# Optimization experiments

Measured on AMD Instinct MI355X. Metric: run time of the kernel, lower is better.

## Reference

```python
import jax, jax.numpy as jnp
import numpy as np

D = 512      # model dim
H = 8        # heads
HD = D // H  # head dim = 64
NQ = 2048    # n_query
NC = 4096    # n_context
EPS = 1e-5   # LayerNorm eps (torch default)


def setup_inputs() -> dict:
    key = jax.random.key(0)
    ks = jax.random.split(key, 12)
    s = 0.02
    return {
        "query_repr": jax.random.normal(ks[0], (NQ, D), dtype=jnp.float32),
        "context_repr": jax.random.normal(ks[1], (NC, D), dtype=jnp.float32),
        "query_coords": jax.random.uniform(ks[2], (NQ, 2), dtype=jnp.float32) * 10.0,
        "context_coords": jax.random.uniform(ks[3], (NC, 2), dtype=jnp.float32) * 10.0,
        "Wq": jax.random.normal(ks[4], (D, D), dtype=jnp.float32) * s,
        "bq": jnp.zeros((D,), jnp.float32),
        "Wk": jax.random.normal(ks[5], (D, D), dtype=jnp.float32) * s,
        "bk": jnp.zeros((D,), jnp.float32),
        "Wv": jax.random.normal(ks[6], (D, D), dtype=jnp.float32) * s,
        "bv": jnp.zeros((D,), jnp.float32),
        "Wo": jax.random.normal(ks[7], (D, D), dtype=jnp.float32) * s,
        "bo": jnp.zeros((D,), jnp.float32),
        "ln_g": jnp.ones((D,), jnp.float32),
        "ln_b": jnp.zeros((D,), jnp.float32),
        "log_scale": jnp.array(0.0, jnp.float32),          # log_distance_scale
        "bias_per_head": jnp.ones((H,), jnp.float32),      # distance_bias_per_head
    }


def reference(query_repr, context_repr, query_coords, context_coords,
              Wq, bq, Wk, bk, Wv, bv, Wo, bo, ln_g, ln_b,
              log_scale, bias_per_head):
    # pairwise Euclidean distances (NQ, NC)
    diff = query_coords[:, None, :] - context_coords[None, :, :]
    dist = jnp.sqrt(jnp.sum(diff * diff, axis=-1))
    # per-head additive attention bias (H, NQ, NC)
    bias = (-jnp.exp(log_scale) * dist)[None, :, :] * bias_per_head[:, None, None]

    # multi-head attention (batch=1, eval mode so dropout is identity)
    q = (query_repr @ Wq.T + bq).reshape(NQ, H, HD).transpose(1, 0, 2)    # (H, NQ, HD)
    k = (context_repr @ Wk.T + bk).reshape(NC, H, HD).transpose(1, 0, 2)  # (H, NC, HD)
    v = (context_repr @ Wv.T + bv).reshape(NC, H, HD).transpose(1, 0, 2)  # (H, NC, HD)

    scale = 1.0 / jnp.sqrt(jnp.float32(HD))
    scores = jnp.einsum('hqd,hkd->hqk', q, k) * scale + bias              # (H, NQ, NC)
    attn = jax.nn.softmax(scores, axis=-1)
    ctx = jnp.einsum('hqk,hkd->hqd', attn, v)                             # (H, NQ, HD)
    attended = ctx.transpose(1, 0, 2).reshape(NQ, D) @ Wo.T + bo          # (NQ, D)

    # residual + LayerNorm
    x = attended + query_repr
    mu = jnp.mean(x, axis=-1, keepdims=True)
    var = jnp.mean((x - mu) ** 2, axis=-1, keepdims=True)
    return (x - mu) / jnp.sqrt(var + EPS) * ln_g + ln_b
```

## Files before the change

kernel.cpp:

```cpp
#include <hip/hip_runtime.h>

#define D 512
#define H 8
#define HD 64
#define NQ 2048
#define NC 4096
#define SPLIT 8
#define CLEN (NC / SPLIT)
#define NT (CLEN / 32)
#define M0 3.0f
#define KP2 136
#define VP 40

#define TBM 128
#define TBN 64
#define TBK 32
#define TPAD 40

typedef __attribute__((ext_vector_type(8))) short short8;
typedef __attribute__((ext_vector_type(4))) short short4v;
typedef __attribute__((ext_vector_type(4))) float float4v;
typedef __attribute__((ext_vector_type(4))) int int4v;

__device__ inline float bf2f(short s) {
    unsigned int u = ((unsigned int)(unsigned short)s) << 16;
    return __builtin_bit_cast(float, u);
}
__device__ inline short f2bf(float f) {
    unsigned int u = __builtin_bit_cast(unsigned int, f);
    u = (u + 0x7FFF + ((u >> 16) & 1)) >> 16;
    return (short)u;
}
__device__ inline int cvtpk(float a, float b) {
    int w;
    asm("v_cvt_pk_bf16_f32 %0, %1, %2" : "=v"(w) : "v"(a), "v"(b));
    return w;
}

__global__ __launch_bounds__(256) void cast_all(
    const float* __restrict__ s0, const float* __restrict__ s1,
    const float* __restrict__ s2, const float* __restrict__ s3,
    const float* __restrict__ s4, const float* __restrict__ s5,
    short* __restrict__ dst)
{
    int i = blockIdx.x * 256 + threadIdx.x;
    const float* src; int off;
    if      (i < 262144) { src = s0; off = i; }
    else if (i < 786432) { src = s1; off = i - 262144; }
    else if (i < 851968) { src = s2; off = i - 786432; }
    else if (i < 917504) { src = s3; off = i - 851968; }
    else if (i < 983040) { src = s4; off = i - 917504; }
    else                 { src = s5; off = i - 983040; }
    float4v v = ((const float4v*)src)[off];
    short4v o;
    o.x = f2bf(v.x); o.y = f2bf(v.y); o.z = f2bf(v.z); o.w = f2bf(v.w);
    ((short4v*)dst)[i] = o;
}

__global__ __launch_bounds__(256) void gemm_bt_bias(
    const short* __restrict__ X, const short* __restrict__ W,
    const float* __restrict__ bias, short* __restrict__ out, int M)
{
    int wave = threadIdx.x >> 6, lane = threadIdx.x & 63;
    int gt = blockIdx.x * 4 + wave;
    int tm = gt >> 3;
    int tg = gt & 7;
    if (tm >= (M >> 4)) return;
    int l15 = lane & 15, quad = lane >> 4;
    const short* xp = X + (tm * 16 + l15) * D + quad * 8;
    const short* wp = W + (tg * 64 + l15) * D + quad * 8;
    float4v a0 = {0,0,0,0}, a1 = {0,0,0,0}, a2 = {0,0,0,0}, a3 = {0,0,0,0};
#pragma unroll
    for (int k = 0; k < D; k += 32) {
        short8 a  = *(const short8*)(xp + k);
        short8 b0 = *(const short8*)(wp + k);
        short8 b1 = *(const short8*)(wp + 16 * D + k);
        short8 b2 = *(const short8*)(wp + 32 * D + k);
        short8 b3 = *(const short8*)(wp + 48 * D + k);
        a0 = __builtin_amdgcn_mfma_f32_16x16x32_bf16(a, b0, a0, 0, 0, 0);
        a1 = __builtin_amdgcn_mfma_f32_16x16x32_bf16(a, b1, a1, 0, 0, 0);
        a2 = __builtin_amdgcn_mfma_f32_16x16x32_bf16(a, b2, a2, 0, 0, 0);
        a3 = __builtin_amdgcn_mfma_f32_16x16x32_bf16(a, b3, a3, 0, 0, 0);
    }
    int orow = tm * 16 + quad * 4;
    float4v accs[4] = {a0, a1, a2, a3};
#pragma unroll
    for (int j = 0; j < 4; j++) {
        int col = tg * 64 + j * 16 + l15;
        float bv = bias[col];
#pragma unroll
        for (int r = 0; r < 4; r++)
            out[(orow + r) * D + col] = f2bf(accs[j][r] + bv);
    }
}

__global__ __launch_bounds__(256) void gemm_qkv_tiled(
    const short* __restrict__ Xq, const short* __restrict__ Xc,
    const short* __restrict__ Wq, const short* __restrict__ Wk,
    const short* __restrict__ Wv,
    const float* __restrict__ bq, const float* __restrict__ bk,
    const float* __restrict__ bv,
    short* __restrict__ Qout, short* __restrict__ Kout,
    short* __restrict__ VoutT)
{
    __shared__ __align__(16) short Ab[2][TBM * TPAD];
    __shared__ __align__(16) short Bb[2][TBN * TPAD];

    int tid = threadIdx.x;
    int wave = tid >> 6, lane = tid & 63;
    int quad = lane >> 4, l15 = lane & 15;

    int blk = blockIdx.x;
    const short *X, *W;
    const float* bias;
    short* outp;
    int bm, bn, vmode;
    if (blk < 128) {
        X = Xq; W = Wq; bias = bq; outp = Qout; vmode = 0;
        bm = (blk >> 3) * TBM; bn = (blk & 7) * TBN;
    } else if (blk < 384) {
        int b = blk - 128;
        X = Xc; W = Wk; bias = bk; outp = Kout; vmode = 0;
        bm = (b >> 3) * TBM; bn = (b & 7) * TBN;
    } else {
        int b = blk - 384;
        X = Xc; W = Wv; bias = bv; outp = VoutT; vmode = 1;
        bm = (b >> 3) * TBM; bn = (b & 7) * TBN;
    }

    int ar = tid >> 1, ac = (tid & 1) * 16;
    int br = tid >> 2, bc = (tid & 3) * 8;
    const short* ag = X + (size_t)(bm + ar) * D + ac;
    const short* bg = W + (size_t)(bn + br) * D + bc;
    short* aw0 = &Ab[0][ar * TPAD + ac];
    short* aw1 = &Ab[1][ar * TPAD + ac];
    short* bw0 = &Bb[0][br * TPAD + bc];
    short* bw1 = &Bb[1][br * TPAD + bc];

    short8 ra0, ra1, rb;

#define GLOAD(ks) { const short* ap_ = ag + (ks) * TBK;                        \
        ra0 = *(const short8*)(ap_);                                           \
        ra1 = *(const short8*)(ap_ + 8);                                       \
        rb  = *(const short8*)(bg + (ks) * TBK); }
#define GDSW0 { *(short8*)aw0 = ra0; *(short8*)(aw0 + 8) = ra1;                \
                *(short8*)bw0 = rb; }
#define GDSW1 { *(short8*)aw1 = ra0; *(short8*)(aw1 + 8) = ra1;                \
                *(short8*)bw1 = rb; }

    float4v c00 = {0,0,0,0}, c01 = {0,0,0,0}, c02 = {0,0,0,0}, c03 = {0,0,0,0};
    float4v c10 = {0,0,0,0}, c11 = {0,0,0,0}, c12 = {0,0,0,0}, c13 = {0,0,0,0};

#define GCOMP(B)                                                               \
    {                                                                          \
        const short* abase = &Ab[B][(wave * 32 + l15) * TPAD + quad * 8];      \
        const short* bbase = &Bb[B][l15 * TPAD + quad * 8];                    \
        short8 a0 = *(const short8*)(abase);                                   \
        short8 a1 = *(const short8*)(abase + 16 * TPAD);                       \
        short8 b0 = *(const short8*)(bbase);                                   \
        short8 b1 = *(const short8*)(bbase + 16 * TPAD);                       \
        short8 b2 = *(const short8*)(bbase + 32 * TPAD);                       \
        short8 b3 = *(const short8*)(bbase + 48 * TPAD);                       \
        c00 = __builtin_amdgcn_mfma_f32_16x16x32_bf16(a0, b0, c00, 0, 0, 0);   \
        c01 = __builtin_amdgcn_mfma_f32_16x16x32_bf16(a0, b1, c01, 0, 0, 0);   \
        c02 = __builtin_amdgcn_mfma_f32_16x16x32_bf16(a0, b2, c02, 0, 0, 0);   \
        c03 = __builtin_amdgcn_mfma_f32_16x16x32_bf16(a0, b3, c03, 0, 0, 0);   \
        c10 = __builtin_amdgcn_mfma_f32_16x16x32_bf16(a1, b0, c10, 0, 0, 0);   \
        c11 = __builtin_amdgcn_mfma_f32_16x16x32_bf16(a1, b1, c11, 0, 0, 0);   \
        c12 = __builtin_amdgcn_mfma_f32_16x16x32_bf16(a1, b2, c12, 0, 0, 0);   \
        c13 = __builtin_amdgcn_mfma_f32_16x16x32_bf16(a1, b3, c13, 0, 0, 0);   \
    }

    GLOAD(0);
    GDSW0;
    GLOAD(1);
    __syncthreads();

    for (int t = 0; t < 14; t += 2) {
        GDSW1;
        GLOAD(t + 2);
        GCOMP(0);
        __syncthreads();
        GDSW0;
        GLOAD(t + 3);
        GCOMP(1);
        __syncthreads();
    }
    GDSW1;
    GCOMP(0);
    __syncthreads();
    GCOMP(1);

#undef GLOAD
#undef GDSW0
#undef GDSW1
#undef GCOMP

    float4v accs[2][4] = {{c00, c01, c02, c03}, {c10, c11, c12, c13}};
    if (vmode == 0) {
#pragma unroll
        for (int mf = 0; mf < 2; mf++) {
            int orow = bm + wave * 32 + mf * 16 + quad * 4;
#pragma unroll
            for (int nf = 0; nf < 4; nf++) {
                int col = bn + nf * 16 + l15;
                float bb_ = bias[col];
#pragma unroll
                for (int r = 0; r < 4; r++)
                    outp[(size_t)(orow + r) * D + col] = f2bf(accs[mf][nf][r] + bb_);
            }
        }
    } else {
#pragma unroll
        for (int mf = 0; mf < 2; mf++) {
            int orow = bm + wave * 32 + mf * 16 + quad * 4;
            int a = (orow & 31) >> 2;
            int posb = (a < 4) ? (8 * a) : (8 * (a - 4) + 4);
            int cp = (orow & ~31) + posb;
#pragma unroll
            for (int nf = 0; nf < 4; nf++) {
                int col = bn + nf * 16 + l15;
                float bb_ = bias[col];
                short4v o;
#pragma unroll
                for (int r = 0; r < 4; r++) o[r] = f2bf(accs[mf][nf][r] + bb_);
                *(short4v*)(outp + (size_t)col * NC + cp) = o;
            }
        }
    }
}

__global__ __launch_bounds__(256) void gemm_res_ln(
    const short* __restrict__ X, const short* __restrict__ W,
    const float* __restrict__ bias, const float* __restrict__ resid,
    const float* __restrict__ g, const float* __restrict__ b,
    float* __restrict__ out)
{
    __shared__ float redS[4][4][4];
    __shared__ float redV[4][4][4];

    int wave = threadIdx.x >> 6, lane = threadIdx.x & 63;
    int l15 = lane & 15, quad = lane >> 4;
    int tm = blockIdx.x;
    const short* xp  = X + (tm * 16 + l15) * D + quad * 8;
    const short* wp0 = W + ((2 * wave) * 64 + l15) * D + quad * 8;
    const short* wp1 = wp0 + 64 * D;
    float4v a00 = {0,0,0,0}, a01 = {0,0,0,0}, a02 = {0,0,0,0}, a03 = {0,0,0,0};
    float4v a10 = {0,0,0,0}, a11 = {0,0,0,0}, a12 = {0,0,0,0}, a13 = {0,0,0,0};
#pragma unroll
    for (int k = 0; k < D; k += 32) {
        short8 a   = *(const short8*)(xp + k);
        short8 b00 = *(const short8*)(wp0 + k);
        short8 b01 = *(const short8*)(wp0 + 16 * D + k);
        short8 b02 = *(const short8*)(wp0 + 32 * D + k);
        short8 b03 = *(const short8*)(wp0 + 48 * D + k);
        short8 b10 = *(const short8*)(wp1 + k);
        short8 b11 = *(const short8*)(wp1 + 16 * D + k);
        short8 b12 = *(const short8*)(wp1 + 32 * D + k);
        short8 b13 = *(const short8*)(wp1 + 48 * D + k);
        a00 = __builtin_amdgcn_mfma_f32_16x16x32_bf16(a, b00, a00, 0, 0, 0);
        a01 = __builtin_amdgcn_mfma_f32_16x16x32_bf16(a, b01, a01, 0, 0, 0);
        a02 = __builtin_amdgcn_mfma_f32_16x16x32_bf16(a, b02, a02, 0, 0, 0);
        a03 = __builtin_amdgcn_mfma_f32_16x16x32_bf16(a, b03, a03, 0, 0, 0);
        a10 = __builtin_amdgcn_mfma_f32_16x16x32_bf16(a, b10, a10, 0, 0, 0);
        a11 = __builtin_amdgcn_mfma_f32_16x16x32_bf16(a, b11, a11, 0, 0, 0);
        a12 = __builtin_amdgcn_mfma_f32_16x16x32_bf16(a, b12, a12, 0, 0, 0);
        a13 = __builtin_amdgcn_mfma_f32_16x16x32_bf16(a, b13, a13, 0, 0, 0);
    }
    int orow = tm * 16 + quad * 4;
    float v[2][4][4];
    float4v accs[2][4] = {{a00, a01, a02, a03}, {a10, a11, a12, a13}};
#pragma unroll
    for (int t = 0; t < 2; t++) {
#pragma unroll
        for (int j = 0; j < 4; j++) {
            int col = (2 * wave + t) * 64 + j * 16 + l15;
            float bv = bias[col];
#pragma unroll
            for (int r = 0; r < 4; r++)
                v[t][j][r] = accs[t][j][r] + bv + resid[(orow + r) * D + col];
        }
    }
    float ps[4];
#pragma unroll
    for (int r = 0; r < 4; r++) {
        float s = 0.f;
#pragma unroll
        for (int t = 0; t < 2; t++)
#pragma unroll
            for (int j = 0; j < 4; j++) s += v[t][j][r];
#pragma unroll
        for (int off = 1; off < 16; off <<= 1) s += __shfl_xor(s, off);
        ps[r] = s;
    }
    if (l15 == 0) {
#pragma unroll
        for (int r = 0; r < 4; r++) redS[wave][quad][r] = ps[r];
    }
    __syncthreads();
    float mu[4];
#pragma unroll
    for (int r = 0; r < 4; r++)
        mu[r] = (redS[0][quad][r] + redS[1][quad][r] +
                 redS[2][quad][r] + redS[3][quad][r]) * (1.f / D);
#pragma unroll
    for (int r = 0; r < 4; r++) {
        float s = 0.f;
#pragma unroll
        for (int t = 0; t < 2; t++)
#pragma unroll
            for (int j = 0; j < 4; j++) {
                float d = v[t][j][r] - mu[r];
                s += d * d;
            }
#pragma unroll
        for (int off = 1; off < 16; off <<= 1) s += __shfl_xor(s, off);
        ps[r] = s;
    }
    if (l15 == 0) {
#pragma unroll
        for (int r = 0; r < 4; r++) redV[wave][quad][r] = ps[r];
    }
    __syncthreads();
    float rstd[4];
#pragma unroll
    for (int r = 0; r < 4; r++) {
        float var = (redV[0][quad][r] + redV[1][quad][r] +
                     redV[2][quad][r] + redV[3][quad][r]) * (1.f / D);
        rstd[r] = rsqrtf(var + 1e-5f);
    }
#pragma unroll
    for (int t = 0; t < 2; t++) {
#pragma unroll
        for (int j = 0; j < 4; j++) {
            int col = (2 * wave + t) * 64 + j * 16 + l15;
            float gc = g[col], bc = b[col];
#pragma unroll
            for (int r = 0; r < 4; r++)
                out[(orow + r) * D + col] =
                    (v[t][j][r] - mu[r]) * rstd[r] * gc + bc;
        }
    }
}

__global__ __launch_bounds__(256) void gemm_bt_bias_res_f32(
    const short* __restrict__ X, const short* __restrict__ W,
    const float* __restrict__ bias, const float* __restrict__ resid,
    float* __restrict__ out, int M)
{
    int wave = threadIdx.x >> 6, lane = threadIdx.x & 63;
    int gt = blockIdx.x * 4 + wave;
    int tm = gt >> 3;
    int tg = gt & 7;
    if (tm >= (M >> 4)) return;
    int l15 = lane & 15, quad = lane >> 4;
    const short* xp = X + (tm * 16 + l15) * D + quad * 8;
    const short* wp = W + (tg * 64 + l15) * D + quad * 8;
    float4v a0 = {0,0,0,0}, a1 = {0,0,0,0}, a2 = {0,0,0,0}, a3 = {0,0,0,0};
#pragma unroll
    for (int k = 0; k < D; k += 32) {
        short8 a  = *(const short8*)(xp + k);
        short8 b0 = *(const short8*)(wp + k);
        short8 b1 = *(const short8*)(wp + 16 * D + k);
        short8 b2 = *(const short8*)(wp + 32 * D + k);
        short8 b3 = *(const short8*)(wp + 48 * D + k);
        a0 = __builtin_amdgcn_mfma_f32_16x16x32_bf16(a, b0, a0, 0, 0, 0);
        a1 = __builtin_amdgcn_mfma_f32_16x16x32_bf16(a, b1, a1, 0, 0, 0);
        a2 = __builtin_amdgcn_mfma_f32_16x16x32_bf16(a, b2, a2, 0, 0, 0);
        a3 = __builtin_amdgcn_mfma_f32_16x16x32_bf16(a, b3, a3, 0, 0, 0);
    }
    int orow = tm * 16 + quad * 4;
    float4v accs[4] = {a0, a1, a2, a3};
#pragma unroll
    for (int j = 0; j < 4; j++) {
        int col = tg * 64 + j * 16 + l15;
        float bv = bias[col];
#pragma unroll
        for (int r = 0; r < 4; r++) {
            int q = orow + r;
            out[q * D + col] = accs[j][r] + bv + resid[q * D + col];
        }
    }
}

__global__ __launch_bounds__(256) void attn_mfma_split9(
    const short* __restrict__ Q, const short* __restrict__ K,
    const short* __restrict__ Vp,
    const float* __restrict__ qc, const float* __restrict__ cc,
    const float* __restrict__ log_scale, const float* __restrict__ bph,
    short* __restrict__ Opart, float* __restrict__ Lpart)
{
    __shared__ __align__(16) short Klds[2][32 * KP2];
    __shared__ __align__(16) short Vlds[2][128 * VP];
    __shared__ __align__(16) float ccl[512];

    int tid = threadIdx.x;
    int wave = tid >> 6, lane = tid & 63;
    int h0 = blockIdx.y * 2;
    int sp = blockIdx.z;
    int q0 = blockIdx.x * 64 + wave * 16;
    int quad = lane >> 4, l15 = lane & 15;
    int cbase = sp * CLEN;

    const float LOG2E = 1.4426950408889634f;
    const float escale = 0.125f * LOG2E;
    const float M0L = M0 * LOG2E;
    float ebase = __expf(log_scale[0]);
    float bh0 = ebase * bph[h0] * LOG2E;
    float bh1 = ebase * bph[h0 + 1] * LOG2E;

    const short* qp = Q + (q0 + l15) * D + h0 * HD + quad * 8;
    short8 qa0_0 = *(const short8*)(qp);
    short8 qa1_0 = *(const short8*)(qp + 32);
    short8 qa0_1 = *(const short8*)(qp + 64);
    short8 qa1_1 = *(const short8*)(qp + 96);

    float qx = qc[(q0 + l15) * 2];
    float qy = qc[(q0 + l15) * 2 + 1];

    float lacc0 = 0.f, lacc1 = 0.f;
    float4v O00 = {0,0,0,0}, O01 = {0,0,0,0}, O02 = {0,0,0,0}, O03 = {0,0,0,0};
    float4v O10 = {0,0,0,0}, O11 = {0,0,0,0}, O12 = {0,0,0,0}, O13 = {0,0,0,0};

    int kr_ = tid >> 3, kc_ = tid & 7;
    int vr_ = tid >> 2, vc_ = tid & 3;
    const short* kg  = K + (size_t)h0 * HD + kc_ * 8;
    const short* vg0 = Vp + (size_t)(h0 * HD + vr_) * NC + vc_ * 8;
    const short* vg1 = Vp + (size_t)(h0 * HD + 64 + vr_) * NC + vc_ * 8;
    short* kw0a = &Klds[0][kr_ * KP2 + kc_ * 8];
    short* kw1a = &Klds[1][kr_ * KP2 + kc_ * 8];
    short* vw0a = &Vlds[0][vr_ * VP + vc_ * 8];
    short* vw0b = &Vlds[0][(64 + vr_) * VP + vc_ * 8];
    short* vw1a = &Vlds[1][vr_ * VP + vc_ * 8];
    short* vw1b = &Vlds[1][(64 + vr_) * VP + vc_ * 8];

    short8 rka, rkb, rva, rvb;

#define LOADR(c0_)                                                             \
    {                                                                          \
        const short* kp_ = kg + (size_t)((c0_) + kr_) * D;                     \
        rka = *(const short8*)(kp_);                                           \
        rkb = *(const short8*)(kp_ + 64);                                      \
        rva = *(const short8*)(vg0 + (c0_));                                   \
        rvb = *(const short8*)(vg1 + (c0_));                                   \
    }

#define DSW0 { *(short8*)kw0a = rka; *(short8*)(kw0a + 64) = rkb;              \
               *(short8*)vw0a = rva; *(short8*)vw0b = rvb; }
#define DSW1 { *(short8*)kw1a = rka; *(short8*)(kw1a + 64) = rkb;              \
               *(short8*)vw1a = rva; *(short8*)vw1b = rvb; }

    const float2* ccp = (const float2*)ccl;

#define HEAD(hoff, QA0, QA1, BH, LACC, OA, OB, OC, OD)                         \
    {                                                                          \
        short8 k00 = *(const short8*)(kb + l15 * KP2 + (hoff) + quad * 8);     \
        short8 k01 = *(const short8*)(kb + l15 * KP2 + (hoff) + 32 + quad * 8);\
        short8 k10 = *(const short8*)(kb + (16 + l15) * KP2 + (hoff) + quad * 8);\
        short8 k11 = *(const short8*)(kb + (16 + l15) * KP2 + (hoff) + 32 + quad * 8);\
        float4v s0 = {0,0,0,0}, s1 = {0,0,0,0};                                \
        s0 = __builtin_amdgcn_mfma_f32_16x16x32_bf16(k00, QA0, s0, 0, 0, 0);   \
        s0 = __builtin_amdgcn_mfma_f32_16x16x32_bf16(k01, QA1, s0, 0, 0, 0);   \
        s1 = __builtin_amdgcn_mfma_f32_16x16x32_bf16(k10, QA0, s1, 0, 0, 0);   \
        s1 = __builtin_amdgcn_mfma_f32_16x16x32_bf16(k11, QA1, s1, 0, 0, 0);   \
        short8 v0 = *(const short8*)(vb + ((hoff) / 64 * 64 + l15) * VP + quad * 8);       \
        short8 v1 = *(const short8*)(vb + ((hoff) / 64 * 64 + 16 + l15) * VP + quad * 8);  \
        short8 v2 = *(const short8*)(vb + ((hoff) / 64 * 64 + 32 + l15) * VP + quad * 8);  \
        short8 v3 = *(const short8*)(vb + ((hoff) / 64 * 64 + 48 + l15) * VP + quad * 8);  \
        float p00 = exp2f(__fmaf_rn(s0[0], escale, __fmaf_rn(-(BH), dA0, -M0L)));\
        float p01 = exp2f(__fmaf_rn(s0[1], escale, __fmaf_rn(-(BH), dA1, -M0L)));\
        float p02 = exp2f(__fmaf_rn(s0[2], escale, __fmaf_rn(-(BH), dA2, -M0L)));\
        float p03 = exp2f(__fmaf_rn(s0[3], escale, __fmaf_rn(-(BH), dA3, -M0L)));\
        float p10 = exp2f(__fmaf_rn(s1[0], escale, __fmaf_rn(-(BH), dB0, -M0L)));\
        float p11 = exp2f(__fmaf_rn(s1[1], escale, __fmaf_rn(-(BH), dB1, -M0L)));\
        float p12 = exp2f(__fmaf_rn(s1[2], escale, __fmaf_rn(-(BH), dB2, -M0L)));\
        float p13 = exp2f(__fmaf_rn(s1[3], escale, __fmaf_rn(-(BH), dB3, -M0L)));\
        LACC += ((p00 + p01) + (p02 + p03)) + ((p10 + p11) + (p12 + p13));     \
        int4v pw;                                                              \
        pw.x = cvtpk(p00, p01); pw.y = cvtpk(p02, p03);                        \
        pw.z = cvtpk(p10, p11); pw.w = cvtpk(p12, p13);                        \
        short8 pa = __builtin_bit_cast(short8, pw);                            \
        OA = __builtin_amdgcn_mfma_f32_16x16x32_bf16(pa, v0, OA, 0, 0, 0);     \
        OB = __builtin_amdgcn_mfma_f32_16x16x32_bf16(pa, v1, OB, 0, 0, 0);     \
        OC = __builtin_amdgcn_mfma_f32_16x16x32_bf16(pa, v2, OC, 0, 0, 0);     \
        OD = __builtin_amdgcn_mfma_f32_16x16x32_bf16(pa, v3, OD, 0, 0, 0);     \
    }

#define COMPUTE_TILE(B, lo)                                                    \
    {                                                                          \
        const short* kb = &Klds[B][0];                                         \
        const short* vb = &Vlds[B][0];                                         \
        float2 ca0 = ccp[(lo) + 4 * quad + 0], cb0 = ccp[(lo) + 16 + 4 * quad + 0];\
        float2 ca1 = ccp[(lo) + 4 * quad + 1], cb1 = ccp[(lo) + 16 + 4 * quad + 1];\
        float2 ca2 = ccp[(lo) + 4 * quad + 2], cb2 = ccp[(lo) + 16 + 4 * quad + 2];\
        float2 ca3 = ccp[(lo) + 4 * quad + 3], cb3 = ccp[(lo) + 16 + 4 * quad + 3];\
        float dx, dy;                                                          \
        dx = qx - ca0.x; dy = qy - ca0.y;                                      \
        float dA0 = __builtin_amdgcn_sqrtf(__fmaf_rn(dx, dx, dy * dy));        \
        dx = qx - ca1.x; dy = qy - ca1.y;                                      \
        float dA1 = __builtin_amdgcn_sqrtf(__fmaf_rn(dx, dx, dy * dy));        \
        dx = qx - ca2.x; dy = qy - ca2.y;                                      \
        float dA2 = __builtin_amdgcn_sqrtf(__fmaf_rn(dx, dx, dy * dy));        \
        dx = qx - ca3.x; dy = qy - ca3.y;                                      \
        float dA3 = __builtin_amdgcn_sqrtf(__fmaf_rn(dx, dx, dy * dy));        \
        dx = qx - cb0.x; dy = qy - cb0.y;                                      \
        float dB0 = __builtin_amdgcn_sqrtf(__fmaf_rn(dx, dx, dy * dy));        \
        dx = qx - cb1.x; dy = qy - cb1.y;                                      \
        float dB1 = __builtin_amdgcn_sqrtf(__fmaf_rn(dx, dx, dy * dy));        \
        dx = qx - cb2.x; dy = qy - cb2.y;                                      \
        float dB2 = __builtin_amdgcn_sqrtf(__fmaf_rn(dx, dx, dy * dy));        \
        dx = qx - cb3.x; dy = qy - cb3.y;                                      \
        float dB3 = __builtin_amdgcn_sqrtf(__fmaf_rn(dx, dx, dy * dy));        \
        HEAD(0,  qa0_0, qa1_0, bh0, lacc0, O00, O01, O02, O03)                 \
        HEAD(64, qa0_1, qa1_1, bh1, lacc1, O10, O11, O12, O13)                 \
    }

    ((float2*)ccl)[tid] = ((const float2*)cc)[cbase + tid];
    LOADR(cbase);
    DSW0;
    LOADR(cbase + 32);
    __syncthreads();

    for (int t = 0; t < NT - 2; t += 2) {
        int c0 = cbase + t * 32;
        if (t == 8) {
            ((float2*)ccl)[tid] = ((const float2*)cc)[cbase + 256 + tid];
            __syncthreads();
        }
        DSW1;
        LOADR(c0 + 64);
        COMPUTE_TILE(0, (t & 7) * 32);
        __syncthreads();
        DSW0;
        LOADR(c0 + 96);
        COMPUTE_TILE(1, (t & 7) * 32 + 32);
        __syncthreads();
    }
    DSW1;
    COMPUTE_TILE(0, 192);
    __syncthreads();
    COMPUTE_TILE(1, 224);

#undef LOADR
#undef DSW0
#undef DSW1
#undef HEAD
#undef COMPUTE_TILE

    lacc0 += __shfl_xor(lacc0, 16);
    lacc0 += __shfl_xor(lacc0, 32);
    lacc1 += __shfl_xor(lacc1, 16);
    lacc1 += __shfl_xor(lacc1, 32);

    long base0 = (long)(sp * H + h0) * NQ;
    long base1 = base0 + NQ;
    float4v Oarr0[4] = {O00, O01, O02, O03};
    float4v Oarr1[4] = {O10, O11, O12, O13};
#pragma unroll
    for (int t = 0; t < 4; t++) {
#pragma unroll
        for (int r = 0; r < 4; r++) {
            int q = q0 + quad * 4 + r;
            Opart[(base0 + q) * HD + t * 16 + l15] = f2bf(Oarr0[t][r]);
            Opart[(base1 + q) * HD + t * 16 + l15] = f2bf(Oarr1[t][r]);
        }
    }
    if (lane < 16) {
        Lpart[base0 + q0 + lane] = lacc0;
        Lpart[base1 + q0 + lane] = lacc1;
    }
}

__global__ __launch_bounds__(256) void attn_combine(
    const short* __restrict__ Opart, const float* __restrict__ Lpart,
    short* __restrict__ Att)
{
    int id = blockIdx.x * 256 + threadIdx.x;
    int d = id & 63;
    int q = (id >> 6) & (NQ - 1);
    int h = id >> 17;
    float L = 0.f, acc = 0.f;
#pragma unroll
    for (int s = 0; s < SPLIT; s++) {
        long b = (long)(s * H + h) * NQ + q;
        L   += Lpart[b];
        acc += bf2f(Opart[b * HD + d]);
    }
    Att[q * D + h * HD + d] = f2bf(acc / L);
}

__global__ __launch_bounds__(256) void attn_mfma(
    const short* __restrict__ Q, const short* __restrict__ K,
    const short* __restrict__ V,
    const float* __restrict__ qc, const float* __restrict__ cc,
    const float* __restrict__ log_scale, const float* __restrict__ bph,
    short* __restrict__ out)
{
    __shared__ short Vt[HD][48];
    __shared__ short P[4][16][48];
    int wave = threadIdx.x >> 6, lane = threadIdx.x & 63;
    int h = blockIdx.y;
    int q0 = blockIdx.x * 64 + wave * 16;
    int quad = lane >> 4, l15 = lane & 15;
    const float scale = 0.125f;
    float bh = __expf(log_scale[0]) * bph[h];
    const short* qp = Q + (q0 + l15) * D + h * HD + quad * 8;
    short8 qa0 = *(const short8*)(qp);
    short8 qa1 = *(const short8*)(qp + 32);
    float qx[4], qy[4];
#pragma unroll
    for (int r = 0; r < 4; r++) {
        int q = q0 + quad * 4 + r;
        qx[r] = qc[q * 2]; qy[r] = qc[q * 2 + 1];
    }
    float m[4], l[4];
    float4v O[4];
#pragma unroll
    for (int r = 0; r < 4; r++) { m[r] = -1e30f; l[r] = 0.f; }
#pragma unroll
    for (int t = 0; t < 4; t++) O[t] = (float4v){0.f, 0.f, 0.f, 0.f};
    for (int c0 = 0; c0 < NC; c0 += 32) {
        __syncthreads();
        {
            int c = threadIdx.x >> 3;
            int dblk = (threadIdx.x & 7) * 8;
            short8 vv = *(const short8*)(V + (c0 + c) * D + h * HD + dblk);
#pragma unroll
            for (int j = 0; j < 8; j++) Vt[dblk + j][c] = vv[j];
        }
        const short* kp0 = K + (c0 + l15) * D + h * HD + quad * 8;
        const short* kp1 = kp0 + 16 * D;
        short8 kb00 = *(const short8*)(kp0);
        short8 kb01 = *(const short8*)(kp0 + 32);
        short8 kb10 = *(const short8*)(kp1);
        short8 kb11 = *(const short8*)(kp1 + 32);
        float4v s0 = {0,0,0,0}, s1 = {0,0,0,0};
        s0 = __builtin_amdgcn_mfma_f32_16x16x32_bf16(qa0, kb00, s0, 0, 0, 0);
        s0 = __builtin_amdgcn_mfma_f32_16x16x32_bf16(qa1, kb01, s0, 0, 0, 0);
        s1 = __builtin_amdgcn_mfma_f32_16x16x32_bf16(qa0, kb10, s1, 0, 0, 0);
        s1 = __builtin_amdgcn_mfma_f32_16x16x32_bf16(qa1, kb11, s1, 0, 0, 0);
        int cA = c0 + l15, cB = cA + 16;
        float cxA = cc[cA * 2], cyA = cc[cA * 2 + 1];
        float cxB = cc[cB * 2], cyB = cc[cB * 2 + 1];
#pragma unroll
        for (int r = 0; r < 4; r++) {
            float dxA = qx[r] - cxA, dyA = qy[r] - cyA;
            float dxB = qx[r] - cxB, dyB = qy[r] - cyB;
            float v0 = s0[r] * scale - bh * sqrtf(dxA * dxA + dyA * dyA);
            float v1 = s1[r] * scale - bh * sqrtf(dxB * dxB + dyB * dyB);
            float mx = fmaxf(v0, v1);
#pragma unroll
            for (int off = 1; off < 16; off <<= 1) mx = fmaxf(mx, __shfl_xor(mx, off));
            float mnew = fmaxf(m[r], mx);
            float alpha = __expf(m[r] - mnew);
            float p0 = __expf(v0 - mnew);
            float p1 = __expf(v1 - mnew);
            float ps = p0 + p1;
#pragma unroll
            for (int off = 1; off < 16; off <<= 1) ps += __shfl_xor(ps, off);
            l[r] = l[r] * alpha + ps;
            m[r] = mnew;
#pragma unroll
            for (int t = 0; t < 4; t++) O[t][r] *= alpha;
            P[wave][quad * 4 + r][l15]      = f2bf(p0);
            P[wave][quad * 4 + r][16 + l15] = f2bf(p1);
        }
        __syncthreads();
        short8 pa = *(const short8*)(&P[wave][l15][quad * 8]);
#pragma unroll
        for (int t = 0; t < 4; t++) {
            short8 vb = *(const short8*)(&Vt[t * 16 + l15][quad * 8]);
            O[t] = __builtin_amdgcn_mfma_f32_16x16x32_bf16(pa, vb, O[t], 0, 0, 0);
        }
    }
#pragma unroll
    for (int t = 0; t < 4; t++) {
#pragma unroll
        for (int r = 0; r < 4; r++) {
            int q = q0 + quad * 4 + r;
            out[q * D + h * HD + t * 16 + l15] = f2bf(O[t][r] / l[r]);
        }
    }
}

__global__ __launch_bounds__(256) void layernorm_kernel(
    const float* __restrict__ X, const float* __restrict__ g,
    const float* __restrict__ b, float* __restrict__ out)
{
    int wave = threadIdx.x >> 6, lane = threadIdx.x & 63;
    int row = blockIdx.x * 4 + wave;
    const float* xp = X + row * D;
    float v[8];
    float s = 0.f;
#pragma unroll
    for (int i = 0; i < 8; i++) { v[i] = xp[lane + i * 64]; s += v[i]; }
#pragma unroll
    for (int off = 1; off < 64; off <<= 1) s += __shfl_xor(s, off);
    float mu = s * (1.f / D);
    float var = 0.f;
#pragma unroll
    for (int i = 0; i < 8; i++) { float d = v[i] - mu; var += d * d; }
#pragma unroll
    for (int off = 1; off < 64; off <<= 1) var += __shfl_xor(var, off);
    float rstd = rsqrtf(var * (1.f / D) + 1e-5f);
#pragma unroll
    for (int i = 0; i < 8; i++) {
        int c = lane + i * 64;
        out[row * D + c] = (v[i] - mu) * rstd * g[c] + b[c];
    }
}

extern "C" void kernel_launch(void* const* d_in, const int* in_sizes, int n_in,
                              void* d_out, int out_size, void* d_ws, size_t ws_size,
                              hipStream_t stream) {
    const float* query_repr     = (const float*)d_in[0];
    const float* context_repr   = (const float*)d_in[1];
    const float* query_coords   = (const float*)d_in[2];
    const float* context_coords = (const float*)d_in[3];
    const float* Wq = (const float*)d_in[4];
    const float* bq = (const float*)d_in[5];
    const float* Wk = (const float*)d_in[6];
    const float* bk = (const float*)d_in[7];
    const float* Wv = (const float*)d_in[8];
    const float* bv = (const float*)d_in[9];
    const float* Wo = (const float*)d_in[10];
    const float* bo = (const float*)d_in[11];
    const float* ln_g = (const float*)d_in[12];
    const float* ln_b = (const float*)d_in[13];
    const float* log_scale = (const float*)d_in[14];
    const float* bph = (const float*)d_in[15];

    short* ws = (short*)d_ws;
    short* Xq_bf = ws;
    short* Xc_bf = Xq_bf + NQ * D;
    short* Wq_bf = Xc_bf + NC * D;
    short* Wk_bf = Wq_bf + D * D;
    short* Wv_bf = Wk_bf + D * D;
    short* Wo_bf = Wv_bf + D * D;
    short* Qw  = Wo_bf + D * D;
    short* Kw  = Qw + NQ * D;
    short* Vw  = Kw + NC * D;
    short* Att = Vw + NC * D;
    float* Xf  = (float*)(Att + NQ * D);
    short* Opart = (short*)(Xf + NQ * D);
    float* Lpart = (float*)(Opart + (size_t)SPLIT * H * NQ * HD);
    size_t ws_needed_split = ((char*)(Lpart + (size_t)SPLIT * H * NQ)) - (char*)d_ws;

    cast_all<<<dim3(4096), 256, 0, stream>>>(
        query_repr, context_repr, Wq, Wk, Wv, Wo, Xq_bf);

    if (ws_size >= ws_needed_split) {
        gemm_qkv_tiled<<<dim3(640), 256, 0, stream>>>(
            Xq_bf, Xc_bf, Wq_bf, Wk_bf, Wv_bf, bq, bk, bv, Qw, Kw, Vw);
        attn_mfma_split9<<<dim3(NQ / 64, H / 2, SPLIT), 256, 0, stream>>>(
            Qw, Kw, Vw, query_coords, context_coords, log_scale, bph,
            Opart, Lpart);
        attn_combine<<<dim3(H * NQ * HD / 256), 256, 0, stream>>>(
            Opart, Lpart, Att);
        gemm_res_ln<<<dim3(NQ / 16), 256, 0, stream>>>(
            Att, Wo_bf, bo, query_repr, ln_g, ln_b, (float*)d_out);
    } else {
        gemm_bt_bias<<<dim3((NQ / 16) * 8 / 4), 256, 0, stream>>>(
            Xq_bf, Wq_bf, bq, Qw, NQ);
        gemm_bt_bias<<<dim3((NC / 16) * 8 / 4), 256, 0, stream>>>(
            Xc_bf, Wk_bf, bk, Kw, NC);
        gemm_bt_bias<<<dim3((NC / 16) * 8 / 4), 256, 0, stream>>>(
            Xc_bf, Wv_bf, bv, Vw, NC);
        attn_mfma<<<dim3(NQ / 64, H), 256, 0, stream>>>(
            Qw, Kw, Vw, query_coords, context_coords, log_scale, bph, Att);
        gemm_bt_bias_res_f32<<<dim3((NQ / 16) * 8 / 4), 256, 0, stream>>>(
            Att, Wo_bf, bo, query_repr, Xf, NQ);
        layernorm_kernel<<<dim3(NQ / 4), 256, 0, stream>>>(
            Xf, ln_g, ln_b, (float*)d_out);
    }
}
```

Measured before the change: 173.7 us.

## Replace fused out-proj+LayerNorm with LDS-tiled double-buffered GEMM plus separate LayerNorm

```diff
diff --git a/kernel.cpp b/kernel.cpp
--- a/kernel.cpp
+++ b/kernel.cpp
@@ -230,115 +230,101 @@
     }
 }
 
-__global__ __launch_bounds__(256) void gemm_res_ln(
+__global__ __launch_bounds__(256) void gemm_out_tiled(
     const short* __restrict__ X, const short* __restrict__ W,
     const float* __restrict__ bias, const float* __restrict__ resid,
-    const float* __restrict__ g, const float* __restrict__ b,
     float* __restrict__ out)
 {
-    __shared__ float redS[4][4][4];
-    __shared__ float redV[4][4][4];
-
-    int wave = threadIdx.x >> 6, lane = threadIdx.x & 63;
-    int l15 = lane & 15, quad = lane >> 4;
-    int tm = blockIdx.x;
-    const short* xp  = X + (tm * 16 + l15) * D + quad * 8;
-    const short* wp0 = W + ((2 * wave) * 64 + l15) * D + quad * 8;
-    const short* wp1 = wp0 + 64 * D;
-    float4v a00 = {0,0,0,0}, a01 = {0,0,0,0}, a02 = {0,0,0,0}, a03 = {0,0,0,0};
-    float4v a10 = {0,0,0,0}, a11 = {0,0,0,0}, a12 = {0,0,0,0}, a13 = {0,0,0,0};
-#pragma unroll
-    for (int k = 0; k < D; k += 32) {
-        short8 a   = *(const short8*)(xp + k);
-        short8 b00 = *(const short8*)(wp0 + k);
-        short8 b01 = *(const short8*)(wp0 + 16 * D + k);
-        short8 b02 = *(const short8*)(wp0 + 32 * D + k);
-        short8 b03 = *(const short8*)(wp0 + 48 * D + k);
-        short8 b10 = *(const short8*)(wp1 + k);
-        short8 b11 = *(const short8*)(wp1 + 16 * D + k);
-        short8 b12 = *(const short8*)(wp1 + 32 * D + k);
-        short8 b13 = *(const short8*)(wp1 + 48 * D + k);
-        a00 = __builtin_amdgcn_mfma_f32_16x16x32_bf16(a, b00, a00, 0, 0, 0);
-        a01 = __builtin_amdgcn_mfma_f32_16x16x32_bf16(a, b01, a01, 0, 0, 0);
-        a02 = __builtin_amdgcn_mfma_f32_16x16x32_bf16(a, b02, a02, 0, 0, 0);
-        a03 = __builtin_amdgcn_mfma_f32_16x16x32_bf16(a, b03, a03, 0, 0, 0);
-        a10 = __builtin_amdgcn_mfma_f32_16x16x32_bf16(a, b10, a10, 0, 0, 0);
-        a11 = __builtin_amdgcn_mfma_f32_16x16x32_bf16(a, b11, a11, 0, 0, 0);
-        a12 = __builtin_amdgcn_mfma_f32_16x16x32_bf16(a, b12, a12, 0, 0, 0);
-        a13 = __builtin_amdgcn_mfma_f32_16x16x32_bf16(a, b13, a13, 0, 0, 0);
-    }
-    int orow = tm * 16 + quad * 4;
-    float v[2][4][4];
-    float4v accs[2][4] = {{a00, a01, a02, a03}, {a10, a11, a12, a13}};
-#pragma unroll
-    for (int t = 0; t < 2; t++) {
-#pragma unroll
-        for (int j = 0; j < 4; j++) {
-            int col = (2 * wave + t) * 64 + j * 16 + l15;
-            float bv = bias[col];
+    __shared__ __align__(16) short Ab[2][TBM * TPAD];
+    __shared__ __align__(16) short Bb[2][TBN * TPAD];
+
+    int tid = threadIdx.x;
+    int wave = tid >> 6, lane = tid & 63;
+    int quad = lane >> 4, l15 = lane & 15;
+
+    int blk = blockIdx.x;
+    int bm = (blk >> 3) * TBM, bn = (blk & 7) * TBN;
+
+    int ar = tid >> 1, ac = (tid & 1) * 16;
+    int br = tid >> 2, bc = (tid & 3) * 8;
+    const short* ag = X + (size_t)(bm + ar) * D + ac;
+    const short* bg = W + (size_t)(bn + br) * D + bc;
+    short* aw0 = &Ab[0][ar * TPAD + ac];
+    short* aw1 = &Ab[1][ar * TPAD + ac];
+    short* bw0 = &Bb[0][br * TPAD + bc];
+    short* bw1 = &Bb[1][br * TPAD + bc];
+
+    short8 ra0, ra1, rb;
+
+#define GLOAD(ks) { const short* ap_ = ag + (ks) * TBK;                        \
+        ra0 = *(const short8*)(ap_);                                           \
+        ra1 = *(const short8*)(ap_ + 8);                                       \
+        rb  = *(const short8*)(bg + (ks) * TBK); }
+#define GDSW0 { *(short8*)aw0 = ra0; *(short8*)(aw0 + 8) = ra1;                \
+                *(short8*)bw0 = rb; }
+#define GDSW1 { *(short8*)aw1 = ra0; *(short8*)(aw1 + 8) = ra1;                \
+                *(short8*)bw1 = rb; }
+
+    float4v c00 = {0,0,0,0}, c01 = {0,0,0,0}, c02 = {0,0,0,0}, c03 = {0,0,0,0};
+    float4v c10 = {0,0,0,0}, c11 = {0,0,0,0}, c12 = {0,0,0,0}, c13 = {0,0,0,0};
+
+#define GCOMP(B)                                                               \
+    {                                                                          \
+        const short* abase = &Ab[B][(wave * 32 + l15) * TPAD + quad * 8];      \
+        const short* bbase = &Bb[B][l15 * TPAD + quad * 8];                    \
+        short8 a0 = *(const short8*)(abase);                                   \
+        short8 a1 = *(const short8*)(abase + 16 * TPAD);                       \
+        short8 b0 = *(const short8*)(bbase);                                   \
+        short8 b1 = *(const short8*)(bbase + 16 * TPAD);                       \
+        short8 b2 = *(const short8*)(bbase + 32 * TPAD);                       \
+        short8 b3 = *(const short8*)(bbase + 48 * TPAD);                       \
+        c00 = __builtin_amdgcn_mfma_f32_16x16x32_bf16(a0, b0, c00, 0, 0, 0);   \
+        c01 = __builtin_amdgcn_mfma_f32_16x16x32_bf16(a0, b1, c01, 0, 0, 0);   \
+        c02 = __builtin_amdgcn_mfma_f32_16x16x32_bf16(a0, b2, c02, 0, 0, 0);   \
+        c03 = __builtin_amdgcn_mfma_f32_16x16x32_bf16(a0, b3, c03, 0, 0, 0);   \
+        c10 = __builtin_amdgcn_mfma_f32_16x16x32_bf16(a1, b0, c10, 0, 0, 0);   \
+        c11 = __builtin_amdgcn_mfma_f32_16x16x32_bf16(a1, b1, c11, 0, 0, 0);   \
+        c12 = __builtin_amdgcn_mfma_f32_16x16x32_bf16(a1, b2, c12, 0, 0, 0);   \
+        c13 = __builtin_amdgcn_mfma_f32_16x16x32_bf16(a1, b3, c13, 0, 0, 0);   \
+    }
+
+    GLOAD(0);
+    GDSW0;
+    GLOAD(1);
+    __syncthreads();
+
+    for (int t = 0; t < 14; t += 2) {
+        GDSW1;
+        GLOAD(t + 2);
+        GCOMP(0);
+        __syncthreads();
+        GDSW0;
+        GLOAD(t + 3);
+        GCOMP(1);
+        __syncthreads();
+    }
+    GDSW1;
+    GCOMP(0);
+    __syncthreads();
+    GCOMP(1);
+
+#undef GLOAD
+#undef GDSW0
+#undef GDSW1
+#undef GCOMP
+
+    float4v accs[2][4] = {{c00, c01, c02, c03}, {c10, c11, c12, c13}};
+#pragma unroll
+    for (int mf = 0; mf < 2; mf++) {
+        int orow = bm + wave * 32 + mf * 16 + quad * 4;
+#pragma unroll
+        for (int nf = 0; nf < 4; nf++) {
+            int col = bn + nf * 16 + l15;
+            float bb_ = bias[col];
 #pragma unroll
             for (int r = 0; r < 4; r++)
-                v[t][j][r] = accs[t][j][r] + bv + resid[(orow + r) * D + col];
-        }
-    }
-    float ps[4];
-#pragma unroll
-    for (int r = 0; r < 4; r++) {
-        float s = 0.f;
-#pragma unroll
-        for (int t = 0; t < 2; t++)
-#pragma unroll
-            for (int j = 0; j < 4; j++) s += v[t][j][r];
-#pragma unroll
-        for (int off = 1; off < 16; off <<= 1) s += __shfl_xor(s, off);
-        ps[r] = s;
-    }
-    if (l15 == 0) {
-#pragma unroll
-        for (int r = 0; r < 4; r++) redS[wave][quad][r] = ps[r];
-    }
-    __syncthreads();
-    float mu[4];
-#pragma unroll
-    for (int r = 0; r < 4; r++)
-        mu[r] = (redS[0][quad][r] + redS[1][quad][r] +
-                 redS[2][quad][r] + redS[3][quad][r]) * (1.f / D);
-#pragma unroll
-    for (int r = 0; r < 4; r++) {
-        float s = 0.f;
-#pragma unroll
-        for (int t = 0; t < 2; t++)
-#pragma unroll
-            for (int j = 0; j < 4; j++) {
-                float d = v[t][j][r] - mu[r];
-                s += d * d;
-            }
-#pragma unroll
-        for (int off = 1; off < 16; off <<= 1) s += __shfl_xor(s, off);
-        ps[r] = s;
-    }
-    if (l15 == 0) {
-#pragma unroll
-        for (int r = 0; r < 4; r++) redV[wave][quad][r] = ps[r];
-    }
-    __syncthreads();
-    float rstd[4];
-#pragma unroll
-    for (int r = 0; r < 4; r++) {
-        float var = (redV[0][quad][r] + redV[1][quad][r] +
-                     redV[2][quad][r] + redV[3][quad][r]) * (1.f / D);
-        rstd[r] = rsqrtf(var + 1e-5f);
-    }
-#pragma unroll
-    for (int t = 0; t < 2; t++) {
-#pragma unroll
-        for (int j = 0; j < 4; j++) {
-            int col = (2 * wave + t) * 64 + j * 16 + l15;
-            float gc = g[col], bc = b[col];
-#pragma unroll
-            for (int r = 0; r < 4; r++)
-                out[(orow + r) * D + col] =
-                    (v[t][j][r] - mu[r]) * rstd[r] * gc + bc;
+                out[(size_t)(orow + r) * D + col] =
+                    accs[mf][nf][r] + bb_ + resid[(size_t)(orow + r) * D + col];
         }
     }
 }
@@ -757,8 +743,10 @@
             Opart, Lpart);
         attn_combine<<<dim3(H * NQ * HD / 256), 256, 0, stream>>>(
             Opart, Lpart, Att);
-        gemm_res_ln<<<dim3(NQ / 16), 256, 0, stream>>>(
-            Att, Wo_bf, bo, query_repr, ln_g, ln_b, (float*)d_out);
+        gemm_out_tiled<<<dim3(128), 256, 0, stream>>>(
+            Att, Wo_bf, bo, query_repr, Xf);
+        layernorm_kernel<<<dim3(NQ / 4), 256, 0, stream>>>(
+            Xf, ln_g, ln_b, (float*)d_out);
     } else {
         gemm_bt_bias<<<dim3((NQ / 16) * 8 / 4), 256, 0, stream>>>(
             Xq_bf, Wq_bf, bq, Qw, NQ);
```

Result: faster. 170.0 us (-2.1%).
